# Performance work log

Hardware: AMD Instinct MI355X
Metric: run time of the kernel (lower is better)

Reference implementation:

```python
import jax, jax.numpy as jnp
import numpy as np

N_NODES = 100000
N_EDGES = 3200000
D_IN = 256
D_OUT = 256


def setup_inputs() -> dict:
    key = jax.random.key(0)
    k1, k2, k3, k4, k5 = jax.random.split(key, 5)
    x = jax.random.normal(k1, (N_NODES, D_IN), dtype=jnp.float32)
    weight = jax.random.normal(k2, (D_IN, D_OUT), dtype=jnp.float32) * (1.0 / np.sqrt(D_IN))
    edge_row = jax.random.randint(k3, (N_EDGES,), 0, N_NODES, dtype=jnp.int32)
    edge_col = jax.random.randint(k4, (N_EDGES,), 0, N_NODES, dtype=jnp.int32)
    edge_val = jax.random.uniform(k5, (N_EDGES,), dtype=jnp.float32)
    return {"x": x, "weight": weight, "edge_row": edge_row,
            "edge_col": edge_col, "edge_val": edge_val}


def reference(x, weight, edge_row, edge_col, edge_val):
    # support = dropout(x) @ W  (dropout p=0 -> identity, eval-mode math)
    support = x @ weight                       # [N, D_OUT]
    # output = spmm(adj, support): for each edge (r, c, v): out[r] += v * support[c]
    gathered = edge_val[:, None] * support[edge_col]   # [E, D_OUT]
    output = jax.ops.segment_sum(gathered, edge_row, num_segments=N_NODES)
    return output
```

## Files before the change

### kernel.cpp

```cpp
#include <hip/hip_runtime.h>

#define N_NODES 100000
#define N_EDGES 3200000
#define DIM 256

typedef _Float16 half_t;
typedef __attribute__((ext_vector_type(4))) _Float16 half4;
typedef __attribute__((ext_vector_type(8))) _Float16 half8;
typedef __attribute__((ext_vector_type(4))) float floatx4;
typedef __attribute__((ext_vector_type(4))) int intx4;

__global__ __launch_bounds__(256) void castw_kernel(const float* __restrict__ w,
                                                    half_t* __restrict__ wT) {
    __shared__ float tile[32][33];
    int bk = blockIdx.x * 32;
    int bn = blockIdx.y * 32;
    int tx = threadIdx.x & 31, ty = threadIdx.x >> 5;
#pragma unroll
    for (int i = 0; i < 4; i++)
        tile[ty + i * 8][tx] = w[(size_t)(bk + ty + i * 8) * DIM + bn + tx];
    __syncthreads();
#pragma unroll
    for (int i = 0; i < 4; i++)
        wT[(size_t)(bn + ty + i * 8) * DIM + bk + tx] = (half_t)tile[tx][ty + i * 8];
}

#define BM 128
#define BK 32
#define LDK 40

__global__ __launch_bounds__(512) void gemm_f16_kernel(const float* __restrict__ A,
                                                       const half_t* __restrict__ BT,
                                                       half_t* __restrict__ C, int M) {
    __shared__ half_t As[BM][LDK];
    __shared__ half_t Bs[256][LDK];

    const int tid = threadIdx.x;
    const int wid = tid >> 6, lane = tid & 63;
    const int wm = wid & 1, wn = wid >> 1;
    const int row0 = blockIdx.x * BM;
    const int lr = lane & 15;
    const int quad = lane >> 4;

    floatx4 acc[4][4] = {};

    const int ar = tid >> 2;
    const int ac = (tid & 3) * 8;
    const bool avalid = (row0 + ar) < M;
    const float* aptr = A + (size_t)(row0 + ar) * DIM + ac;

    for (int k0 = 0; k0 < DIM; k0 += BK) {
        {
            const floatx4* src = (const floatx4*)(aptr + k0);
            half_t* dst = &As[ar][ac];
#pragma unroll
            for (int i = 0; i < 2; i++) {
                floatx4 v = avalid ? __builtin_nontemporal_load(src + i)
                                   : (floatx4){0.f, 0.f, 0.f, 0.f};
                half4 h;
                h.x = (half_t)v.x; h.y = (half_t)v.y;
                h.z = (half_t)v.z; h.w = (half_t)v.w;
                ((half4*)dst)[i] = h;
            }
        }
        {
#pragma unroll
            for (int i = 0; i < 2; i++) {
                int ch = tid + i * 512;
                int r = ch >> 2, cb = (ch & 3) * 8;
                half8 v = *(const half8*)(BT + (size_t)r * DIM + k0 + cb);
                *(half8*)&Bs[r][cb] = v;
            }
        }
        __syncthreads();

        half8 a[4], b[4];
#pragma unroll
        for (int i = 0; i < 4; i++)
            a[i] = *(const half8*)&As[wm * 64 + i * 16 + lr][quad * 8];
#pragma unroll
        for (int j = 0; j < 4; j++)
            b[j] = *(const half8*)&Bs[wn * 64 + j * 16 + lr][quad * 8];
#pragma unroll
        for (int i = 0; i < 4; i++)
#pragma unroll
            for (int j = 0; j < 4; j++)
                acc[i][j] = __builtin_amdgcn_mfma_f32_16x16x32_f16(a[i], b[j], acc[i][j], 0, 0, 0);
        __syncthreads();
    }

#pragma unroll
    for (int i = 0; i < 4; i++) {
#pragma unroll
        for (int j = 0; j < 4; j++) {
            int gc = wn * 64 + j * 16 + lr;
            int grb = row0 + wm * 64 + i * 16 + quad * 4;
#pragma unroll
            for (int r = 0; r < 4; r++) {
                int gr = grb + r;
                if (gr < M) C[(size_t)gr * DIM + gc] = (half_t)acc[i][j][r];
            }
        }
    }
}

#define NBUCK 391
#define CAP 16384
#define EPB 4096
#define NEB ((N_EDGES + EPB - 1) / EPB)

__global__ __launch_bounds__(256) void bucket_scatter_kernel(const int* __restrict__ erow,
                                                             const int* __restrict__ ecol,
                                                             const float* __restrict__ eval,
                                                             int* __restrict__ bcursor,
                                                             int2* __restrict__ tmp) {
    __shared__ int lh[NBUCK];
    __shared__ int lbase[NBUCK];
    for (int b = threadIdx.x; b < NBUCK; b += 256) lh[b] = 0;
    __syncthreads();

    int base4 = blockIdx.x * (EPB / 4);
#pragma unroll
    for (int i = 0; i < 4; i++) {
        int idx4 = base4 + i * 256 + threadIdx.x;
        if (idx4 < N_EDGES / 4) {
            intx4 r4 = __builtin_nontemporal_load((const intx4*)erow + idx4);
            atomicAdd(&lh[r4.x >> 8], 1);
            atomicAdd(&lh[r4.y >> 8], 1);
            atomicAdd(&lh[r4.z >> 8], 1);
            atomicAdd(&lh[r4.w >> 8], 1);
        }
    }
    __syncthreads();
    for (int b = threadIdx.x; b < NBUCK; b += 256) {
        int c = lh[b];
        lbase[b] = c ? (b * CAP + atomicAdd(&bcursor[b * 16], c)) : 0;
        lh[b] = 0;
    }
    __syncthreads();

#define SCAT(R, C, V)                                                     \
    {                                                                     \
        int _r = (R), _c = (C);                                           \
        int _b = _r >> 8;                                                 \
        int _rank = atomicAdd(&lh[_b], 1);                                \
        tmp[lbase[_b] + _rank] =                                          \
            make_int2(((_r & 255) << 17) | _c, __float_as_int(V));        \
    }
#pragma unroll
    for (int i = 0; i < 4; i++) {
        int idx4 = base4 + i * 256 + threadIdx.x;
        if (idx4 < N_EDGES / 4) {
            intx4 r4 = __builtin_nontemporal_load((const intx4*)erow + idx4);
            intx4 c4 = __builtin_nontemporal_load((const intx4*)ecol + idx4);
            floatx4 v4 = __builtin_nontemporal_load((const floatx4*)eval + idx4);
            SCAT(r4.x, c4.x, v4.x);
            SCAT(r4.y, c4.y, v4.y);
            SCAT(r4.z, c4.z, v4.z);
            SCAT(r4.w, c4.w, v4.w);
        }
    }
#undef SCAT
}

__global__ __launch_bounds__(512) void scan_buckets_kernel(const int* __restrict__ bcnt,
                                                           int* __restrict__ bbase,
                                                           int* __restrict__ offsets) {
    __shared__ int s[512];
    int t = threadIdx.x;
    int v = (t < NBUCK) ? bcnt[t * 16] : 0;
    s[t] = v;
    __syncthreads();
    for (int off = 1; off < 512; off <<= 1) {
        int u = (t >= off) ? s[t - off] : 0;
        __syncthreads();
        s[t] += u;
        __syncthreads();
    }
    if (t < NBUCK) bbase[t] = s[t] - v;
    if (t == 0) { bbase[NBUCK] = N_EDGES; offsets[N_NODES] = N_EDGES; }
}

__global__ __launch_bounds__(256) void bucket_to_csr_kernel(const int2* __restrict__ tmp,
                                                            const int* __restrict__ bcnt,
                                                            const int* __restrict__ bbase,
                                                            int* __restrict__ offsets,
                                                            int2* __restrict__ sedge) {
    __shared__ int lh[256];
    __shared__ int s[256];
    const int b = blockIdx.x;
    const int t = threadIdx.x;
    const int cnt = bcnt[b * 16];
    const int obase = bbase[b];
    const int2* src = tmp + (size_t)b * CAP;

    lh[t] = 0;
    __syncthreads();
    for (int e = t; e < cnt; e += 256)
        atomicAdd(&lh[src[e].x >> 17], 1);
    __syncthreads();

    int c = lh[t];
    s[t] = c;
    __syncthreads();
    for (int off = 1; off < 256; off <<= 1) {
        int u = (t >= off) ? s[t - off] : 0;
        __syncthreads();
        s[t] += u;
        __syncthreads();
    }
    int ex = s[t] - c;
    int row = (b << 8) + t;
    if (row < N_NODES) offsets[row] = obase + ex;
    lh[t] = ex;
    __syncthreads();

    for (int e = t; e < cnt; e += 256) {
        int2 q = src[e];
        int lr = q.x >> 17;
        int rank = atomicAdd(&lh[lr], 1);
        sedge[obase + rank] = make_int2(q.x & 0x1FFFF, q.y);
    }
}

__global__ __launch_bounds__(256, 8) void spmm_kernel(const half_t* __restrict__ support,
                                                      const int* __restrict__ offsets,
                                                      const int2* __restrict__ edges,
                                                      float* __restrict__ out) {
    int row = (blockIdx.x * blockDim.x + threadIdx.x) >> 6;
    if (row >= N_NODES) return;
    int lane = threadIdx.x & 63;
    int h = lane >> 5;
    int j = lane & 31;

    int beg = offsets[row];
    int end = offsets[row + 1];

    float acc[8] = {0.f, 0.f, 0.f, 0.f, 0.f, 0.f, 0.f, 0.f};
    int e = beg;

    if ((e & 1) && e < end) {
        int2 q0 = edges[e];
        half8 s0 = *(const half8*)(support + (size_t)q0.x * DIM + j * 8);
        float v0 = (h == 0) ? __int_as_float(q0.y) : 0.f;
#pragma unroll
        for (int d = 0; d < 8; d++) acc[d] += v0 * (float)s0[d];
        e++;
    }

    for (; e + 15 < end; e += 16) {
        intx4 pa = __builtin_nontemporal_load((const intx4*)(edges + e + 2 * h));
        intx4 pb = __builtin_nontemporal_load((const intx4*)(edges + e + 4 + 2 * h));
        intx4 pc = __builtin_nontemporal_load((const intx4*)(edges + e + 8 + 2 * h));
        intx4 pd = __builtin_nontemporal_load((const intx4*)(edges + e + 12 + 2 * h));
        half8 s0 = *(const half8*)(support + (size_t)pa.x * DIM + j * 8);
        half8 s1 = *(const half8*)(support + (size_t)pa.z * DIM + j * 8);
        half8 s2 = *(const half8*)(support + (size_t)pb.x * DIM + j * 8);
        half8 s3 = *(const half8*)(support + (size_t)pb.z * DIM + j * 8);
        half8 s4 = *(const half8*)(support + (size_t)pc.x * DIM + j * 8);
        half8 s5 = *(const half8*)(support + (size_t)pc.z * DIM + j * 8);
        half8 s6 = *(const half8*)(support + (size_t)pd.x * DIM + j * 8);
        half8 s7 = *(const half8*)(support + (size_t)pd.z * DIM + j * 8);
        float v0 = __int_as_float(pa.y), v1 = __int_as_float(pa.w);
        float v2 = __int_as_float(pb.y), v3 = __int_as_float(pb.w);
        float v4 = __int_as_float(pc.y), v5 = __int_as_float(pc.w);
        float v6 = __int_as_float(pd.y), v7 = __int_as_float(pd.w);
#pragma unroll
        for (int d = 0; d < 8; d++)
            acc[d] += v0 * (float)s0[d] + v1 * (float)s1[d]
                    + v2 * (float)s2[d] + v3 * (float)s3[d]
                    + v4 * (float)s4[d] + v5 * (float)s5[d]
                    + v6 * (float)s6[d] + v7 * (float)s7[d];
    }
    for (; e + 1 < end; e += 2) {
        int2 q0 = edges[e + h];
        half8 s0 = *(const half8*)(support + (size_t)q0.x * DIM + j * 8);
        float v0 = __int_as_float(q0.y);
#pragma unroll
        for (int d = 0; d < 8; d++) acc[d] += v0 * (float)s0[d];
    }
    if (e < end) {
        int2 q0 = edges[e];
        half8 s0 = *(const half8*)(support + (size_t)q0.x * DIM + j * 8);
        float v0 = (h == 0) ? __int_as_float(q0.y) : 0.f;
#pragma unroll
        for (int d = 0; d < 8; d++) acc[d] += v0 * (float)s0[d];
    }

    float r0, r1, r2, r3, g0, g1, g2, g3;
    if (h == 0) {
        r0 = acc[0]; r1 = acc[1]; r2 = acc[2]; r3 = acc[3];
        g0 = acc[4]; g1 = acc[5]; g2 = acc[6]; g3 = acc[7];
    } else {
        r0 = acc[4]; r1 = acc[5]; r2 = acc[6]; r3 = acc[7];
        g0 = acc[0]; g1 = acc[1]; g2 = acc[2]; g3 = acc[3];
    }
    r0 += __shfl_xor(g0, 32, 64);
    r1 += __shfl_xor(g1, 32, 64);
    r2 += __shfl_xor(g2, 32, 64);
    r3 += __shfl_xor(g3, 32, 64);

    floatx4 res = {r0, r1, r2, r3};
    __builtin_nontemporal_store(res, (floatx4*)(out + (size_t)row * DIM + j * 8 + h * 4));
}

extern "C" void kernel_launch(void* const* d_in, const int* in_sizes, int n_in,
                              void* d_out, int out_size, void* d_ws, size_t ws_size,
                              hipStream_t stream) {
    const float* x    = (const float*)d_in[0];
    const float* w    = (const float*)d_in[1];
    const int*   erow = (const int*)d_in[2];
    const int*   ecol = (const int*)d_in[3];
    const float* eval = (const float*)d_in[4];
    float* out = (float*)d_out;

    char* ws = (char*)d_ws;
    half_t* support = (half_t*)ws;
    int*    offsets = (int*)(ws + 51200000);
    int2*   sedge   = (int2*)(ws + 51600128);
    half_t* wT      = (half_t*)(ws + 77200128);
    int*    bcnt    = (int*)(ws + 77331200);
    int*    bbase   = (int*)(ws + 77356224);
    int2*   tmp     = (int2*)d_out;

    hipMemsetAsync(bcnt, 0, NBUCK * 16 * sizeof(int), stream);

    castw_kernel<<<dim3(8, 8), 256, 0, stream>>>(w, wT);

    dim3 ggrid((N_NODES + BM - 1) / BM, 1);
    gemm_f16_kernel<<<ggrid, 512, 0, stream>>>(x, wT, support, N_NODES);

    bucket_scatter_kernel<<<NEB, 256, 0, stream>>>(erow, ecol, eval, bcnt, tmp);
    scan_buckets_kernel<<<1, 512, 0, stream>>>(bcnt, bbase, offsets);
    bucket_to_csr_kernel<<<NBUCK, 256, 0, stream>>>(tmp, bcnt, bbase, offsets, sedge);

    spmm_kernel<<<(N_NODES * 64 + 255) / 256, 256, 0, stream>>>(support, offsets,
                                                                sedge, out);
}
```

Baseline: 611.4 us.

## Split SpMM into two column-half passes with four edge groups per wave

The SpMM now runs as two launches, each covering 128 of the 256 output columns. Within a wave, four groups of 16 lanes each handle a different edge, and the partial sums are combined with two xor-shuffles. Each pass touches only half of every support row, so the gathered working set per pass is smaller and should stay in cache better. The cost is reading the CSR edge list twice and adding a second launch. Separately, the nontemporal load and store builtins across the GEMM, scatter and SpMM kernels are replaced with plain vector accesses.

```diff
diff --git a/kernel.cpp b/kernel.cpp
--- a/kernel.cpp
+++ b/kernel.cpp
@@ -8,7 +8,6 @@
 typedef __attribute__((ext_vector_type(4))) _Float16 half4;
 typedef __attribute__((ext_vector_type(8))) _Float16 half8;
 typedef __attribute__((ext_vector_type(4))) float floatx4;
-typedef __attribute__((ext_vector_type(4))) int intx4;
 
 __global__ __launch_bounds__(256) void castw_kernel(const float* __restrict__ w,
                                                     half_t* __restrict__ wT) {
@@ -51,12 +50,11 @@
 
     for (int k0 = 0; k0 < DIM; k0 += BK) {
         {
-            const floatx4* src = (const floatx4*)(aptr + k0);
+            const float4* src = (const float4*)(aptr + k0);
             half_t* dst = &As[ar][ac];
 #pragma unroll
             for (int i = 0; i < 2; i++) {
-                floatx4 v = avalid ? __builtin_nontemporal_load(src + i)
-                                   : (floatx4){0.f, 0.f, 0.f, 0.f};
+                float4 v = avalid ? src[i] : make_float4(0.f, 0.f, 0.f, 0.f);
                 half4 h;
                 h.x = (half_t)v.x; h.y = (half_t)v.y;
                 h.z = (half_t)v.z; h.w = (half_t)v.w;
@@ -124,7 +122,7 @@
     for (int i = 0; i < 4; i++) {
         int idx4 = base4 + i * 256 + threadIdx.x;
         if (idx4 < N_EDGES / 4) {
-            intx4 r4 = __builtin_nontemporal_load((const intx4*)erow + idx4);
+            int4 r4 = ((const int4*)erow)[idx4];
             atomicAdd(&lh[r4.x >> 8], 1);
             atomicAdd(&lh[r4.y >> 8], 1);
             atomicAdd(&lh[r4.z >> 8], 1);
@@ -151,9 +149,9 @@
     for (int i = 0; i < 4; i++) {
         int idx4 = base4 + i * 256 + threadIdx.x;
         if (idx4 < N_EDGES / 4) {
-            intx4 r4 = __builtin_nontemporal_load((const intx4*)erow + idx4);
-            intx4 c4 = __builtin_nontemporal_load((const intx4*)ecol + idx4);
-            floatx4 v4 = __builtin_nontemporal_load((const floatx4*)eval + idx4);
+            int4 r4 = ((const int4*)erow)[idx4];
+            int4 c4 = ((const int4*)ecol)[idx4];
+            float4 v4 = ((const float4*)eval)[idx4];
             SCAT(r4.x, c4.x, v4.x);
             SCAT(r4.y, c4.y, v4.y);
             SCAT(r4.z, c4.z, v4.z);
@@ -223,16 +221,17 @@
     }
 }
 
-__global__ __launch_bounds__(256, 8) void spmm_kernel(const half_t* __restrict__ support,
-                                                      const int* __restrict__ offsets,
-                                                      const int2* __restrict__ edges,
-                                                      float* __restrict__ out) {
+__global__ __launch_bounds__(256) void spmm_kernel(const half_t* __restrict__ support,
+                                                   const int* __restrict__ offsets,
+                                                   const int2* __restrict__ edges,
+                                                   float* __restrict__ out, int d0) {
     int row = (blockIdx.x * blockDim.x + threadIdx.x) >> 6;
     if (row >= N_NODES) return;
     int lane = threadIdx.x & 63;
-    int h = lane >> 5;
-    int j = lane & 31;
-
+    int g = lane >> 4;
+    int j = lane & 15;
+
+    const half_t* sup = support + d0;
     int beg = offsets[row];
     int end = offsets[row + 1];
 
@@ -240,68 +239,58 @@
     int e = beg;
 
     if ((e & 1) && e < end) {
-        int2 q0 = edges[e];
-        half8 s0 = *(const half8*)(support + (size_t)q0.x * DIM + j * 8);
-        float v0 = (h == 0) ? __int_as_float(q0.y) : 0.f;
-#pragma unroll
-        for (int d = 0; d < 8; d++) acc[d] += v0 * (float)s0[d];
+        int2 q = edges[e];
+        half8 s = *(const half8*)(sup + (size_t)q.x * DIM + j * 8);
+        float v = (g == 0) ? __int_as_float(q.y) : 0.f;
+#pragma unroll
+        for (int d = 0; d < 8; d++) acc[d] += v * (float)s[d];
         e++;
     }
 
     for (; e + 15 < end; e += 16) {
-        intx4 pa = __builtin_nontemporal_load((const intx4*)(edges + e + 2 * h));
-        intx4 pb = __builtin_nontemporal_load((const intx4*)(edges + e + 4 + 2 * h));
-        intx4 pc = __builtin_nontemporal_load((const intx4*)(edges + e + 8 + 2 * h));
-        intx4 pd = __builtin_nontemporal_load((const intx4*)(edges + e + 12 + 2 * h));
-        half8 s0 = *(const half8*)(support + (size_t)pa.x * DIM + j * 8);
-        half8 s1 = *(const half8*)(support + (size_t)pa.z * DIM + j * 8);
-        half8 s2 = *(const half8*)(support + (size_t)pb.x * DIM + j * 8);
-        half8 s3 = *(const half8*)(support + (size_t)pb.z * DIM + j * 8);
-        half8 s4 = *(const half8*)(support + (size_t)pc.x * DIM + j * 8);
-        half8 s5 = *(const half8*)(support + (size_t)pc.z * DIM + j * 8);
-        half8 s6 = *(const half8*)(support + (size_t)pd.x * DIM + j * 8);
-        half8 s7 = *(const half8*)(support + (size_t)pd.z * DIM + j * 8);
+        int4 pa = *(const int4*)(edges + e + 2 * g);
+        int4 pb = *(const int4*)(edges + e + 8 + 2 * g);
+        half8 s0 = *(const half8*)(sup + (size_t)pa.x * DIM + j * 8);
+        half8 s1 = *(const half8*)(sup + (size_t)pa.z * DIM + j * 8);
+        half8 s2 = *(const half8*)(sup + (size_t)pb.x * DIM + j * 8);
+        half8 s3 = *(const half8*)(sup + (size_t)pb.z * DIM + j * 8);
         float v0 = __int_as_float(pa.y), v1 = __int_as_float(pa.w);
         float v2 = __int_as_float(pb.y), v3 = __int_as_float(pb.w);
-        float v4 = __int_as_float(pc.y), v5 = __int_as_float(pc.w);
-        float v6 = __int_as_float(pd.y), v7 = __int_as_float(pd.w);
 #pragma unroll
         for (int d = 0; d < 8; d++)
             acc[d] += v0 * (float)s0[d] + v1 * (float)s1[d]
-                    + v2 * (float)s2[d] + v3 * (float)s3[d]
-                    + v4 * (float)s4[d] + v5 * (float)s5[d]
-                    + v6 * (float)s6[d] + v7 * (float)s7[d];
-    }
-    for (; e + 1 < end; e += 2) {
-        int2 q0 = edges[e + h];
-        half8 s0 = *(const half8*)(support + (size_t)q0.x * DIM + j * 8);
-        float v0 = __int_as_float(q0.y);
-#pragma unroll
-        for (int d = 0; d < 8; d++) acc[d] += v0 * (float)s0[d];
-    }
-    if (e < end) {
-        int2 q0 = edges[e];
-        half8 s0 = *(const half8*)(support + (size_t)q0.x * DIM + j * 8);
-        float v0 = (h == 0) ? __int_as_float(q0.y) : 0.f;
-#pragma unroll
-        for (int d = 0; d < 8; d++) acc[d] += v0 * (float)s0[d];
-    }
-
-    float r0, r1, r2, r3, g0, g1, g2, g3;
-    if (h == 0) {
-        r0 = acc[0]; r1 = acc[1]; r2 = acc[2]; r3 = acc[3];
-        g0 = acc[4]; g1 = acc[5]; g2 = acc[6]; g3 = acc[7];
-    } else {
-        r0 = acc[4]; r1 = acc[5]; r2 = acc[6]; r3 = acc[7];
-        g0 = acc[0]; g1 = acc[1]; g2 = acc[2]; g3 = acc[3];
-    }
-    r0 += __shfl_xor(g0, 32, 64);
-    r1 += __shfl_xor(g1, 32, 64);
-    r2 += __shfl_xor(g2, 32, 64);
-    r3 += __shfl_xor(g3, 32, 64);
-
-    floatx4 res = {r0, r1, r2, r3};
-    __builtin_nontemporal_store(res, (floatx4*)(out + (size_t)row * DIM + j * 8 + h * 4));
+                    + v2 * (float)s2[d] + v3 * (float)s3[d];
+    }
+    if (e + 7 < end) {
+        int4 pa = *(const int4*)(edges + e + 2 * g);
+        half8 s0 = *(const half8*)(sup + (size_t)pa.x * DIM + j * 8);
+        half8 s1 = *(const half8*)(sup + (size_t)pa.z * DIM + j * 8);
+        float v0 = __int_as_float(pa.y), v1 = __int_as_float(pa.w);
+#pragma unroll
+        for (int d = 0; d < 8; d++)
+            acc[d] += v0 * (float)s0[d] + v1 * (float)s1[d];
+        e += 8;
+    }
+    for (; e < end; e++) {
+        int2 q = edges[e];
+        half8 s = *(const half8*)(sup + (size_t)q.x * DIM + j * 8);
+        float v = (g == 0) ? __int_as_float(q.y) : 0.f;
+#pragma unroll
+        for (int d = 0; d < 8; d++) acc[d] += v * (float)s[d];
+    }
+
+#pragma unroll
+    for (int d = 0; d < 8; d++) {
+        acc[d] += __shfl_xor(acc[d], 16, 64);
+        acc[d] += __shfl_xor(acc[d], 32, 64);
+    }
+
+    if (lane < 32) {
+        int hi = lane >> 4;
+        floatx4 res = {acc[hi * 4 + 0], acc[hi * 4 + 1],
+                       acc[hi * 4 + 2], acc[hi * 4 + 3]};
+        *(floatx4*)(out + (size_t)row * DIM + d0 + j * 8 + hi * 4) = res;
+    }
 }
 
 extern "C" void kernel_launch(void* const* d_in, const int* in_sizes, int n_in,
@@ -334,6 +323,7 @@
     scan_buckets_kernel<<<1, 512, 0, stream>>>(bcnt, bbase, offsets);
     bucket_to_csr_kernel<<<NBUCK, 256, 0, stream>>>(tmp, bcnt, bbase, offsets, sedge);
 
-    spmm_kernel<<<(N_NODES * 64 + 255) / 256, 256, 0, stream>>>(support, offsets,
-                                                                sedge, out);
-}
+    int sgrid = (N_NODES * 64 + 255) / 256;
+    spmm_kernel<<<sgrid, 256, 0, stream>>>(support, offsets, sedge, out, 0);
+    spmm_kernel<<<sgrid, 256, 0, stream>>>(support, offsets, sedge, out, 128);
+}
```

Measured after the change: 558.4 us. 8.7% less time.

## Fuse GEMM with edge bucketing and build CSR in LDS inside SpMM

Applied to the files above, without the earlier changes.

The GEMM and the edge bucket-scatter now run as one launch, split by block index, so the two independent stages can overlap. The scan and bucket-to-CSR kernels are removed. Each SpMM block now sorts its own bucket of 200 rows into shared memory, so edges and offsets are no longer written to and read back from global memory. The trade-offs are about 64 KB of LDS per 512-thread block across only 500 blocks, which lowers occupancy and latency hiding for the gather, and a hard per-bucket capacity clamp that assumes evenly spread row indices.

```diff
diff --git a/kernel.cpp b/kernel.cpp
--- a/kernel.cpp
+++ b/kernel.cpp
@@ -8,7 +8,18 @@
 typedef __attribute__((ext_vector_type(4))) _Float16 half4;
 typedef __attribute__((ext_vector_type(8))) _Float16 half8;
 typedef __attribute__((ext_vector_type(4))) float floatx4;
-typedef __attribute__((ext_vector_type(4))) int intx4;
+
+#define BM 128
+#define BK 32
+#define LDK 40
+#define GEMM_BLOCKS 782
+
+#define NBUCK 500
+#define RPB 200
+#define CAPG 8192
+#define STRIDE_I2 25600
+#define EPB 16384
+#define NEB 196
 
 __global__ __launch_bounds__(256) void castw_kernel(const float* __restrict__ w,
                                                     half_t* __restrict__ wT) {
@@ -25,283 +36,267 @@
         wT[(size_t)(bn + ty + i * 8) * DIM + bk + tx] = (half_t)tile[tx][ty + i * 8];
 }
 
-#define BM 128
-#define BK 32
-#define LDK 40
-
-__global__ __launch_bounds__(512) void gemm_f16_kernel(const float* __restrict__ A,
-                                                       const half_t* __restrict__ BT,
-                                                       half_t* __restrict__ C, int M) {
-    __shared__ half_t As[BM][LDK];
-    __shared__ half_t Bs[256][LDK];
-
+__global__ __launch_bounds__(512) void gemm_scatter_kernel(
+        const float* __restrict__ A, const half_t* __restrict__ BT,
+        half_t* __restrict__ C,
+        const int* __restrict__ erow, const int* __restrict__ ecol,
+        const float* __restrict__ eval, int* __restrict__ bcursor,
+        int2* __restrict__ tmp) {
+    __shared__ __align__(16) char smem[30720];
     const int tid = threadIdx.x;
-    const int wid = tid >> 6, lane = tid & 63;
-    const int wm = wid & 1, wn = wid >> 1;
-    const int row0 = blockIdx.x * BM;
-    const int lr = lane & 15;
-    const int quad = lane >> 4;
-
-    floatx4 acc[4][4] = {};
-
-    const int ar = tid >> 2;
-    const int ac = (tid & 3) * 8;
-    const bool avalid = (row0 + ar) < M;
-    const float* aptr = A + (size_t)(row0 + ar) * DIM + ac;
-
-    for (int k0 = 0; k0 < DIM; k0 += BK) {
-        {
-            const floatx4* src = (const floatx4*)(aptr + k0);
-            half_t* dst = &As[ar][ac];
-#pragma unroll
-            for (int i = 0; i < 2; i++) {
-                floatx4 v = avalid ? __builtin_nontemporal_load(src + i)
-                                   : (floatx4){0.f, 0.f, 0.f, 0.f};
-                half4 h;
-                h.x = (half_t)v.x; h.y = (half_t)v.y;
-                h.z = (half_t)v.z; h.w = (half_t)v.w;
-                ((half4*)dst)[i] = h;
-            }
-        }
-        {
-#pragma unroll
-            for (int i = 0; i < 2; i++) {
-                int ch = tid + i * 512;
-                int r = ch >> 2, cb = (ch & 3) * 8;
-                half8 v = *(const half8*)(BT + (size_t)r * DIM + k0 + cb);
-                *(half8*)&Bs[r][cb] = v;
-            }
-        }
-        __syncthreads();
-
-        half8 a[4], b[4];
-#pragma unroll
-        for (int i = 0; i < 4; i++)
-            a[i] = *(const half8*)&As[wm * 64 + i * 16 + lr][quad * 8];
-#pragma unroll
-        for (int j = 0; j < 4; j++)
-            b[j] = *(const half8*)&Bs[wn * 64 + j * 16 + lr][quad * 8];
-#pragma unroll
-        for (int i = 0; i < 4; i++)
+
+    if (blockIdx.x < GEMM_BLOCKS) {
+        half_t (*As)[LDK] = (half_t (*)[LDK])smem;
+        half_t (*Bs)[LDK] = (half_t (*)[LDK])(smem + 10240);
+
+        const int wid = tid >> 6, lane = tid & 63;
+        const int wm = wid & 1, wn = wid >> 1;
+        const int row0 = blockIdx.x * BM;
+        const int lr = lane & 15;
+        const int quad = lane >> 4;
+
+        floatx4 acc[4][4] = {};
+
+        const int ar = tid >> 2;
+        const int ac = (tid & 3) * 8;
+        const bool avalid = (row0 + ar) < N_NODES;
+        const float* aptr = A + (size_t)(row0 + ar) * DIM + ac;
+
+        for (int k0 = 0; k0 < DIM; k0 += BK) {
+            {
+                const float4* src = (const float4*)(aptr + k0);
+                half_t* dst = &As[ar][ac];
+#pragma unroll
+                for (int i = 0; i < 2; i++) {
+                    float4 v = avalid ? src[i] : make_float4(0.f, 0.f, 0.f, 0.f);
+                    half4 h;
+                    h.x = (half_t)v.x; h.y = (half_t)v.y;
+                    h.z = (half_t)v.z; h.w = (half_t)v.w;
+                    ((half4*)dst)[i] = h;
+                }
+            }
+            {
+#pragma unroll
+                for (int i = 0; i < 2; i++) {
+                    int ch = tid + i * 512;
+                    int r = ch >> 2, cb = (ch & 3) * 8;
+                    half8 v = *(const half8*)(BT + (size_t)r * DIM + k0 + cb);
+                    *(half8*)&Bs[r][cb] = v;
+                }
+            }
+            __syncthreads();
+
+            half8 a[4], b[4];
+#pragma unroll
+            for (int i = 0; i < 4; i++)
+                a[i] = *(const half8*)&As[wm * 64 + i * 16 + lr][quad * 8];
 #pragma unroll
             for (int j = 0; j < 4; j++)
-                acc[i][j] = __builtin_amdgcn_mfma_f32_16x16x32_f16(a[i], b[j], acc[i][j], 0, 0, 0);
-        __syncthreads();
-    }
-
-#pragma unroll
-    for (int i = 0; i < 4; i++) {
-#pragma unroll
-        for (int j = 0; j < 4; j++) {
-            int gc = wn * 64 + j * 16 + lr;
-            int grb = row0 + wm * 64 + i * 16 + quad * 4;
-#pragma unroll
-            for (int r = 0; r < 4; r++) {
-                int gr = grb + r;
-                if (gr < M) C[(size_t)gr * DIM + gc] = (half_t)acc[i][j][r];
-            }
-        }
+                b[j] = *(const half8*)&Bs[wn * 64 + j * 16 + lr][quad * 8];
+#pragma unroll
+            for (int i = 0; i < 4; i++)
+#pragma unroll
+                for (int j = 0; j < 4; j++)
+                    acc[i][j] = __builtin_amdgcn_mfma_f32_16x16x32_f16(
+                        a[i], b[j], acc[i][j], 0, 0, 0);
+            __syncthreads();
+        }
+
+#pragma unroll
+        for (int i = 0; i < 4; i++) {
+#pragma unroll
+            for (int j = 0; j < 4; j++) {
+                int gc = wn * 64 + j * 16 + lr;
+                int grb = row0 + wm * 64 + i * 16 + quad * 4;
+#pragma unroll
+                for (int r = 0; r < 4; r++) {
+                    int gr = grb + r;
+                    if (gr < N_NODES) C[(size_t)gr * DIM + gc] = (half_t)acc[i][j][r];
+                }
+            }
+        }
+    } else {
+        int* lh = (int*)smem;
+        int* lbase = lh + NBUCK;
+        const int sb = blockIdx.x - GEMM_BLOCKS;
+
+        for (int b = tid; b < NBUCK; b += 512) lh[b] = 0;
+        __syncthreads();
+
+        int base4 = sb * (EPB / 4);
+#pragma unroll
+        for (int i = 0; i < 8; i++) {
+            int idx4 = base4 + i * 512 + tid;
+            if (idx4 < N_EDGES / 4) {
+                int4 r4 = ((const int4*)erow)[idx4];
+                atomicAdd(&lh[(unsigned)r4.x / RPB], 1);
+                atomicAdd(&lh[(unsigned)r4.y / RPB], 1);
+                atomicAdd(&lh[(unsigned)r4.z / RPB], 1);
+                atomicAdd(&lh[(unsigned)r4.w / RPB], 1);
+            }
+        }
+        __syncthreads();
+        for (int b = tid; b < NBUCK; b += 512) {
+            int c = lh[b];
+            int st = 0;
+            if (c) {
+                st = atomicAdd(&bcursor[b * 16], c);
+                if (st > CAPG - c) st = CAPG - c;
+                if (st < 0) st = 0;
+            }
+            lbase[b] = b * STRIDE_I2 + st;
+            lh[b] = 0;
+        }
+        __syncthreads();
+
+#define SCAT(R, C, V)                                                      \
+        {                                                                  \
+            unsigned _r = (unsigned)(R); int _c = (C);                     \
+            int _b = _r / RPB;                                             \
+            int _rl = _r - _b * RPB;                                       \
+            int _rank = atomicAdd(&lh[_b], 1);                             \
+            tmp[lbase[_b] + _rank] =                                       \
+                make_int2((_rl << 17) | _c, __float_as_int(V));            \
+        }
+#pragma unroll
+        for (int i = 0; i < 8; i++) {
+            int idx4 = base4 + i * 512 + tid;
+            if (idx4 < N_EDGES / 4) {
+                int4 r4 = ((const int4*)erow)[idx4];
+                int4 c4 = ((const int4*)ecol)[idx4];
+                float4 v4 = ((const float4*)eval)[idx4];
+                SCAT(r4.x, c4.x, v4.x);
+                SCAT(r4.y, c4.y, v4.y);
+                SCAT(r4.z, c4.z, v4.z);
+                SCAT(r4.w, c4.w, v4.w);
+            }
+        }
+#undef SCAT
     }
 }
 
-#define NBUCK 391
-#define CAP 16384
-#define EPB 4096
-#define NEB ((N_EDGES + EPB - 1) / EPB)
-
-__global__ __launch_bounds__(256) void bucket_scatter_kernel(const int* __restrict__ erow,
-                                                             const int* __restrict__ ecol,
-                                                             const float* __restrict__ eval,
-                                                             int* __restrict__ bcursor,
-                                                             int2* __restrict__ tmp) {
-    __shared__ int lh[NBUCK];
-    __shared__ int lbase[NBUCK];
-    for (int b = threadIdx.x; b < NBUCK; b += 256) lh[b] = 0;
-    __syncthreads();
-
-    int base4 = blockIdx.x * (EPB / 4);
-#pragma unroll
-    for (int i = 0; i < 4; i++) {
-        int idx4 = base4 + i * 256 + threadIdx.x;
-        if (idx4 < N_EDGES / 4) {
-            intx4 r4 = __builtin_nontemporal_load((const intx4*)erow + idx4);
-            atomicAdd(&lh[r4.x >> 8], 1);
-            atomicAdd(&lh[r4.y >> 8], 1);
-            atomicAdd(&lh[r4.z >> 8], 1);
-            atomicAdd(&lh[r4.w >> 8], 1);
-        }
-    }
-    __syncthreads();
-    for (int b = threadIdx.x; b < NBUCK; b += 256) {
-        int c = lh[b];
-        lbase[b] = c ? (b * CAP + atomicAdd(&bcursor[b * 16], c)) : 0;
-        lh[b] = 0;
-    }
-    __syncthreads();
-
-#define SCAT(R, C, V)                                                     \
-    {                                                                     \
-        int _r = (R), _c = (C);                                           \
-        int _b = _r >> 8;                                                 \
-        int _rank = atomicAdd(&lh[_b], 1);                                \
-        tmp[lbase[_b] + _rank] =                                          \
-            make_int2(((_r & 255) << 17) | _c, __float_as_int(V));        \
-    }
-#pragma unroll
-    for (int i = 0; i < 4; i++) {
-        int idx4 = base4 + i * 256 + threadIdx.x;
-        if (idx4 < N_EDGES / 4) {
-            intx4 r4 = __builtin_nontemporal_load((const intx4*)erow + idx4);
-            intx4 c4 = __builtin_nontemporal_load((const intx4*)ecol + idx4);
-            floatx4 v4 = __builtin_nontemporal_load((const floatx4*)eval + idx4);
-            SCAT(r4.x, c4.x, v4.x);
-            SCAT(r4.y, c4.y, v4.y);
-            SCAT(r4.z, c4.z, v4.z);
-            SCAT(r4.w, c4.w, v4.w);
-        }
-    }
-#undef SCAT
-}
-
-__global__ __launch_bounds__(512) void scan_buckets_kernel(const int* __restrict__ bcnt,
-                                                           int* __restrict__ bbase,
-                                                           int* __restrict__ offsets) {
-    __shared__ int s[512];
-    int t = threadIdx.x;
-    int v = (t < NBUCK) ? bcnt[t * 16] : 0;
-    s[t] = v;
-    __syncthreads();
-    for (int off = 1; off < 512; off <<= 1) {
-        int u = (t >= off) ? s[t - off] : 0;
-        __syncthreads();
-        s[t] += u;
-        __syncthreads();
-    }
-    if (t < NBUCK) bbase[t] = s[t] - v;
-    if (t == 0) { bbase[NBUCK] = N_EDGES; offsets[N_NODES] = N_EDGES; }
-}
-
-__global__ __launch_bounds__(256) void bucket_to_csr_kernel(const int2* __restrict__ tmp,
-                                                            const int* __restrict__ bcnt,
-                                                            const int* __restrict__ bbase,
-                                                            int* __restrict__ offsets,
-                                                            int2* __restrict__ sedge) {
+__global__ __launch_bounds__(512, 4) void csr_spmm_kernel(
+        const half_t* __restrict__ support, const int* __restrict__ bcnt,
+        const int2* __restrict__ tmp, float* __restrict__ out) {
     __shared__ int lh[256];
     __shared__ int s[256];
+    __shared__ int roff[257];
+    __shared__ __align__(16) int2 ledge[CAPG];
+
     const int b = blockIdx.x;
     const int t = threadIdx.x;
-    const int cnt = bcnt[b * 16];
-    const int obase = bbase[b];
-    const int2* src = tmp + (size_t)b * CAP;
-
-    lh[t] = 0;
-    __syncthreads();
-    for (int e = t; e < cnt; e += 256)
+    int cnt = bcnt[b * 16];
+    if (cnt > CAPG) cnt = CAPG;
+    const int2* src = tmp + (size_t)b * STRIDE_I2;
+    const int row0 = b * RPB;
+
+    if (t < 256) lh[t] = 0;
+    __syncthreads();
+    for (int e = t; e < cnt; e += 512)
         atomicAdd(&lh[src[e].x >> 17], 1);
     __syncthreads();
 
-    int c = lh[t];
-    s[t] = c;
+    if (t < 256) s[t] = lh[t];
     __syncthreads();
     for (int off = 1; off < 256; off <<= 1) {
-        int u = (t >= off) ? s[t - off] : 0;
-        __syncthreads();
-        s[t] += u;
-        __syncthreads();
-    }
-    int ex = s[t] - c;
-    int row = (b << 8) + t;
-    if (row < N_NODES) offsets[row] = obase + ex;
-    lh[t] = ex;
-    __syncthreads();
-
-    for (int e = t; e < cnt; e += 256) {
+        int u = 0;
+        if (t < 256 && t >= off) u = s[t - off];
+        __syncthreads();
+        if (t < 256) s[t] += u;
+        __syncthreads();
+    }
+    if (t < 256) {
+        int ex = s[t] - lh[t];
+        roff[t] = ex;
+        lh[t] = ex;
+    }
+    if (t == 0) roff[256] = cnt;
+    __syncthreads();
+
+    for (int e = t; e < cnt; e += 512) {
         int2 q = src[e];
         int lr = q.x >> 17;
         int rank = atomicAdd(&lh[lr], 1);
-        sedge[obase + rank] = make_int2(q.x & 0x1FFFF, q.y);
-    }
-}
-
-__global__ __launch_bounds__(256, 8) void spmm_kernel(const half_t* __restrict__ support,
-                                                      const int* __restrict__ offsets,
-                                                      const int2* __restrict__ edges,
-                                                      float* __restrict__ out) {
-    int row = (blockIdx.x * blockDim.x + threadIdx.x) >> 6;
-    if (row >= N_NODES) return;
-    int lane = threadIdx.x & 63;
-    int h = lane >> 5;
-    int j = lane & 31;
-
-    int beg = offsets[row];
-    int end = offsets[row + 1];
-
-    float acc[8] = {0.f, 0.f, 0.f, 0.f, 0.f, 0.f, 0.f, 0.f};
-    int e = beg;
-
-    if ((e & 1) && e < end) {
-        int2 q0 = edges[e];
-        half8 s0 = *(const half8*)(support + (size_t)q0.x * DIM + j * 8);
-        float v0 = (h == 0) ? __int_as_float(q0.y) : 0.f;
-#pragma unroll
-        for (int d = 0; d < 8; d++) acc[d] += v0 * (float)s0[d];
-        e++;
-    }
-
-    for (; e + 15 < end; e += 16) {
-        intx4 pa = __builtin_nontemporal_load((const intx4*)(edges + e + 2 * h));
-        intx4 pb = __builtin_nontemporal_load((const intx4*)(edges + e + 4 + 2 * h));
-        intx4 pc = __builtin_nontemporal_load((const intx4*)(edges + e + 8 + 2 * h));
-        intx4 pd = __builtin_nontemporal_load((const intx4*)(edges + e + 12 + 2 * h));
-        half8 s0 = *(const half8*)(support + (size_t)pa.x * DIM + j * 8);
-        half8 s1 = *(const half8*)(support + (size_t)pa.z * DIM + j * 8);
-        half8 s2 = *(const half8*)(support + (size_t)pb.x * DIM + j * 8);
-        half8 s3 = *(const half8*)(support + (size_t)pb.z * DIM + j * 8);
-        half8 s4 = *(const half8*)(support + (size_t)pc.x * DIM + j * 8);
-        half8 s5 = *(const half8*)(support + (size_t)pc.z * DIM + j * 8);
-        half8 s6 = *(const half8*)(support + (size_t)pd.x * DIM + j * 8);
-        half8 s7 = *(const half8*)(support + (size_t)pd.z * DIM + j * 8);
-        float v0 = __int_as_float(pa.y), v1 = __int_as_float(pa.w);
-        float v2 = __int_as_float(pb.y), v3 = __int_as_float(pb.w);
-        float v4 = __int_as_float(pc.y), v5 = __int_as_float(pc.w);
-        float v6 = __int_as_float(pd.y), v7 = __int_as_float(pd.w);
-#pragma unroll
-        for (int d = 0; d < 8; d++)
-            acc[d] += v0 * (float)s0[d] + v1 * (float)s1[d]
-                    + v2 * (float)s2[d] + v3 * (float)s3[d]
-                    + v4 * (float)s4[d] + v5 * (float)s5[d]
-                    + v6 * (float)s6[d] + v7 * (float)s7[d];
-    }
-    for (; e + 1 < end; e += 2) {
-        int2 q0 = edges[e + h];
-        half8 s0 = *(const half8*)(support + (size_t)q0.x * DIM + j * 8);
-        float v0 = __int_as_float(q0.y);
-#pragma unroll
-        for (int d = 0; d < 8; d++) acc[d] += v0 * (float)s0[d];
-    }
-    if (e < end) {
-        int2 q0 = edges[e];
-        half8 s0 = *(const half8*)(support + (size_t)q0.x * DIM + j * 8);
-        float v0 = (h == 0) ? __int_as_float(q0.y) : 0.f;
-#pragma unroll
-        for (int d = 0; d < 8; d++) acc[d] += v0 * (float)s0[d];
-    }
-
-    float r0, r1, r2, r3, g0, g1, g2, g3;
-    if (h == 0) {
-        r0 = acc[0]; r1 = acc[1]; r2 = acc[2]; r3 = acc[3];
-        g0 = acc[4]; g1 = acc[5]; g2 = acc[6]; g3 = acc[7];
-    } else {
-        r0 = acc[4]; r1 = acc[5]; r2 = acc[6]; r3 = acc[7];
-        g0 = acc[0]; g1 = acc[1]; g2 = acc[2]; g3 = acc[3];
-    }
-    r0 += __shfl_xor(g0, 32, 64);
-    r1 += __shfl_xor(g1, 32, 64);
-    r2 += __shfl_xor(g2, 32, 64);
-    r3 += __shfl_xor(g3, 32, 64);
-
-    floatx4 res = {r0, r1, r2, r3};
-    __builtin_nontemporal_store(res, (floatx4*)(out + (size_t)row * DIM + j * 8 + h * 4));
+        ledge[rank] = make_int2(q.x & 0x1FFFF, q.y);
+    }
+    __syncthreads();
+
+    const int wid = t >> 6, lane = t & 63;
+    const int h = lane >> 5;
+    const int j = lane & 31;
+
+    for (int r = wid; r < RPB; r += 8) {
+        int row = row0 + r;
+        int beg = roff[r];
+        int end = roff[r + 1];
+
+        float acc[8] = {0.f, 0.f, 0.f, 0.f, 0.f, 0.f, 0.f, 0.f};
+        int e = beg;
+
+        if ((e & 1) && e < end) {
+            int2 q = ledge[e];
+            half8 sv = *(const half8*)(support + (size_t)q.x * DIM + j * 8);
+            float v = (h == 0) ? __int_as_float(q.y) : 0.f;
+#pragma unroll
+            for (int d = 0; d < 8; d++) acc[d] += v * (float)sv[d];
+            e++;
+        }
+
+        for (; e + 15 < end; e += 16) {
+            int4 pa = *(const int4*)&ledge[e + 2 * h];
+            int4 pb = *(const int4*)&ledge[e + 4 + 2 * h];
+            int4 pc = *(const int4*)&ledge[e + 8 + 2 * h];
+            int4 pd = *(const int4*)&ledge[e + 12 + 2 * h];
+            half8 s0 = *(const half8*)(support + (size_t)pa.x * DIM + j * 8);
+            half8 s1 = *(const half8*)(support + (size_t)pa.z * DIM + j * 8);
+            half8 s2 = *(const half8*)(support + (size_t)pb.x * DIM + j * 8);
+            half8 s3 = *(const half8*)(support + (size_t)pb.z * DIM + j * 8);
+            half8 s4 = *(const half8*)(support + (size_t)pc.x * DIM + j * 8);
+            half8 s5 = *(const half8*)(support + (size_t)pc.z * DIM + j * 8);
+            half8 s6 = *(const half8*)(support + (size_t)pd.x * DIM + j * 8);
+            half8 s7 = *(const half8*)(support + (size_t)pd.z * DIM + j * 8);
+            float v0 = __int_as_float(pa.y), v1 = __int_as_float(pa.w);
+            float v2 = __int_as_float(pb.y), v3 = __int_as_float(pb.w);
+            float v4 = __int_as_float(pc.y), v5 = __int_as_float(pc.w);
+            float v6 = __int_as_float(pd.y), v7 = __int_as_float(pd.w);
+#pragma unroll
+            for (int d = 0; d < 8; d++)
+                acc[d] += v0 * (float)s0[d] + v1 * (float)s1[d]
+                        + v2 * (float)s2[d] + v3 * (float)s3[d]
+                        + v4 * (float)s4[d] + v5 * (float)s5[d]
+                        + v6 * (float)s6[d] + v7 * (float)s7[d];
+        }
+        for (; e + 1 < end; e += 2) {
+            int2 q = ledge[e + h];
+            half8 sv = *(const half8*)(support + (size_t)q.x * DIM + j * 8);
+            float v = __int_as_float(q.y);
+#pragma unroll
+            for (int d = 0; d < 8; d++) acc[d] += v * (float)sv[d];
+        }
+        if (e < end) {
+            int2 q = ledge[e];
+            half8 sv = *(const half8*)(support + (size_t)q.x * DIM + j * 8);
+            float v = (h == 0) ? __int_as_float(q.y) : 0.f;
+#pragma unroll
+            for (int d = 0; d < 8; d++) acc[d] += v * (float)sv[d];
+        }
+
+        float r0, r1, r2, r3, g0, g1, g2, g3;
+        if (h == 0) {
+            r0 = acc[0]; r1 = acc[1]; r2 = acc[2]; r3 = acc[3];
+            g0 = acc[4]; g1 = acc[5]; g2 = acc[6]; g3 = acc[7];
+        } else {
+            r0 = acc[4]; r1 = acc[5]; r2 = acc[6]; r3 = acc[7];
+            g0 = acc[0]; g1 = acc[1]; g2 = acc[2]; g3 = acc[3];
+        }
+        r0 += __shfl_xor(g0, 32, 64);
+        r1 += __shfl_xor(g1, 32, 64);
+        r2 += __shfl_xor(g2, 32, 64);
+        r3 += __shfl_xor(g3, 32, 64);
+
+        *(float4*)(out + (size_t)row * DIM + j * 8 + h * 4) =
+            make_float4(r0, r1, r2, r3);
+    }
 }
 
 extern "C" void kernel_launch(void* const* d_in, const int* in_sizes, int n_in,
@@ -316,24 +311,16 @@
 
     char* ws = (char*)d_ws;
     half_t* support = (half_t*)ws;
-    int*    offsets = (int*)(ws + 51200000);
-    int2*   sedge   = (int2*)(ws + 51600128);
-    half_t* wT      = (half_t*)(ws + 77200128);
-    int*    bcnt    = (int*)(ws + 77331200);
-    int*    bbase   = (int*)(ws + 77356224);
+    half_t* wT      = (half_t*)(ws + 51200000);
+    int*    bcnt    = (int*)(ws + 51331072);
     int2*   tmp     = (int2*)d_out;
 
     hipMemsetAsync(bcnt, 0, NBUCK * 16 * sizeof(int), stream);
 
     castw_kernel<<<dim3(8, 8), 256, 0, stream>>>(w, wT);
 
-    dim3 ggrid((N_NODES + BM - 1) / BM, 1);
-    gemm_f16_kernel<<<ggrid, 512, 0, stream>>>(x, wT, support, N_NODES);
-
-    bucket_scatter_kernel<<<NEB, 256, 0, stream>>>(erow, ecol, eval, bcnt, tmp);
-    scan_buckets_kernel<<<1, 512, 0, stream>>>(bcnt, bbase, offsets);
-    bucket_to_csr_kernel<<<NBUCK, 256, 0, stream>>>(tmp, bcnt, bbase, offsets, sedge);
-
-    spmm_kernel<<<(N_NODES * 64 + 255) / 256, 256, 0, stream>>>(support, offsets,
-                                                                sedge, out);
+    gemm_scatter_kernel<<<GEMM_BLOCKS + NEB, 512, 0, stream>>>(
+        x, wT, support, erow, ecol, eval, bcnt, tmp);
+
+    csr_spmm_kernel<<<NBUCK, 512, 0, stream>>>(support, bcnt, tmp, out);
 }
```

After: 566.8 us. 7.3% less time.
